# Optimization experiments

Measured on AMD Instinct MI355X. Metric: run time of the kernel, lower is better.

Reference implementation:

```python
import jax, jax.numpy as jnp
import numpy as np

# Dims: N=batch, C=heads (depthwise channels), H=W=seq_len (square causal map)
N, C, H, W = 2, 16, 2048, 2048
R, S = 6, 11            # kernel: R over out rows (queries), S over cols (keys)
PAD_H, PAD_W = 5, 5     # pad_h = R-1 (causal in h), pad_w = (S-1)//2 (centered in w)


def setup_inputs() -> dict:
    key = jax.random.key(0)
    k1, k2 = jax.random.split(key)
    x = jax.random.normal(k1, (N, C, H, W), dtype=jnp.float32)
    weight = jax.random.normal(k2, (C, R, S), dtype=jnp.float32) * 0.1
    return {"x": x, "weight": weight}


def reference(x, weight):
    # Causal (lower-triangular) mask h >= w, as in the Triton kernels'
    # `in_h >= in_w` / `out_h >= out_w` masking.
    causal_mask = jnp.tril(jnp.ones((H, W), dtype=bool))  # [H, W]

    # Mask input causally (matches bwd_weight masking x with in_h >= in_w).
    xm = jnp.where(causal_mask, x, jnp.zeros((), x.dtype))  # [N,C,H,W]

    # Depthwise cross-correlation:
    #   y[b,c,p,q] = sum_{r,s} w[c,r,s] * xm[b,c, p+r-PAD_H, q+s-PAD_W]
    # Asymmetric padding keeps output HxW: (PAD_H, R-1-PAD_H) in h => causal
    # taps p-(R-1)..p; (PAD_W, S-1-PAD_W) in w => centered taps.
    y = jax.lax.conv_general_dilated(
        xm,
        weight[:, None, :, :],  # [C,1,R,S] OIHW, depthwise via groups=C
        window_strides=(1, 1),
        padding=((PAD_H, R - 1 - PAD_H), (PAD_W, S - 1 - PAD_W)),
        dimension_numbers=("NCHW", "OIHW", "NCHW"),
        feature_group_count=C,
    )

    # Mask output causally (matches bwd_input masking dout with out_h >= out_w).
    return jnp.where(causal_mask, y, jnp.zeros((), y.dtype))
```

## Files before the change

kernel.cpp:

```cpp
#include <hip/hip_runtime.h>
#include <stdint.h>


#define HDIM 2048
#define WDIM 2048
#define CH   16

#define PITCH 88
#define XROWS 69
#define NSL   (XROWS * 20)

typedef float    f32x4 __attribute__((ext_vector_type(4)));
typedef _Float16 f16x8 __attribute__((ext_vector_type(8)));
typedef _Float16 f16x4 __attribute__((ext_vector_type(4)));

__global__ __launch_bounds__(256, 8)
void dwconv_mfma(const float* __restrict__ x, const float* __restrict__ wgt,
                 float* __restrict__ out) {
  const int bx = blockIdx.x, by = blockIdx.y, plane = blockIdx.z;
  const int q0 = bx * 64, p0 = by * 64;
  const int tid = threadIdx.x;
  const size_t pb = (size_t)plane * HDIM * WDIM;
  const float* __restrict__ xp = x + pb;
  float* __restrict__ op = out + pb;

  if (p0 + 63 < q0) {
    const float4 z = make_float4(0.f, 0.f, 0.f, 0.f);
#pragma unroll
    for (int i = 0; i < 4; ++i) {
      int idx = i * 256 + tid;
      int row = idx >> 4, c4 = idx & 15;
      *(float4*)(op + (size_t)(p0 + row) * WDIM + q0 + 4 * c4) = z;
    }
    return;
  }

  __shared__ _Float16 s_x[XROWS * PITCH];

  const bool pure = (bx >= 1) && (bx <= 30) && (p0 >= q0 + 76);
#pragma unroll
  for (int j = 0; j < 6; ++j) {
    int slot = j * 256 + tid;
    if (slot < NSL) {
      int row = slot / 20;
      int c4 = slot - row * 20;
      int ih = p0 - 5 + row;
      int cb = q0 - 8 + 4 * c4;
      float4 v = make_float4(0.f, 0.f, 0.f, 0.f);
      if (pure) {
        v = *(const float4*)(xp + (size_t)ih * WDIM + cb);
      } else if (ih >= 0) {
        bool fullv = (cb >= 0) && (cb + 3 <= ih) && (cb + 3 < WDIM);
        if (fullv) {
          v = *(const float4*)(xp + (size_t)ih * WDIM + cb);
        } else {
          float* vv = &v.x;
#pragma unroll
          for (int e = 0; e < 4; ++e) {
            int iw = cb + e;
            if (iw >= 0 && iw < WDIM && iw <= ih)
              vv[e] = xp[(size_t)ih * WDIM + iw];
          }
        }
      }
      f16x4 h4;
      h4[0] = (_Float16)v.x; h4[1] = (_Float16)v.y;
      h4[2] = (_Float16)v.z; h4[3] = (_Float16)v.w;
      *(f16x4*)&s_x[row * PITCH + 4 * c4] = h4;
    }
  }

  const int lane = tid & 63;
  const int j16 = lane & 15;
  const int wk = lane >> 4;
  const float* __restrict__ wcp = wgt + (plane & (CH - 1)) * 66;
  f16x8 bw[6];
#pragma unroll
  for (int r = 0; r < 6; ++r) {
#pragma unroll
    for (int i = 0; i < 8; ++i) {
      int k = 8 * wk + i;
      int d = k - j16 - 3;
      bw[r][i] = (_Float16)((d >= 0 && d <= 10) ? wcp[r * 11 + d] : 0.f);
    }
  }

  __syncthreads();

  const int wid = tid >> 6;
  f32x4 acc[4];
#pragma unroll
  for (int t = 0; t < 4; ++t) acc[t] = (f32x4){0.f, 0.f, 0.f, 0.f};

#pragma unroll
  for (int t = 0; t < 4; ++t) {
#pragma unroll
    for (int r = 0; r < 6; ++r) {
      int off = (16 * wid + j16 + r) * PITCH + 16 * t + 8 * wk;
      f16x8 ah = *(const f16x8*)&s_x[off];
      acc[t] = __builtin_amdgcn_mfma_f32_16x16x32_f16(ah, bw[r], acc[t], 0, 0, 0);
    }
  }

  const bool needmask = (q0 + 63 > p0);
#pragma unroll
  for (int t = 0; t < 4; ++t) {
    const int q = q0 + 16 * t + j16;
#pragma unroll
    for (int reg = 0; reg < 4; ++reg) {
      const int p = p0 + 16 * wid + 4 * wk + reg;
      float val = acc[t][reg];
      if (needmask && q > p) val = 0.f;
      op[(size_t)p * WDIM + q] = val;
    }
  }
}

extern "C" void kernel_launch(void* const* d_in, const int* in_sizes, int n_in,
                              void* d_out, int out_size, void* d_ws, size_t ws_size,
                              hipStream_t stream) {
  const float* x   = (const float*)d_in[0];
  const float* wgt = (const float*)d_in[1];
  float* out       = (float*)d_out;
  dim3 grid(WDIM / 64, HDIM / 64, 2 * CH);
  dwconv_mfma<<<grid, dim3(256), 0, stream>>>(x, wgt, out);
}
```

Before: 319.5 us.

## Process both batch planes per block, swap MFMA operands for float4 stores

Each block now handles the same channel for both batch elements. It stages two input tiles into shared memory and reuses the per-channel weight fragments, which halves the grid. The MFMA operands are swapped (weights as A, input as B), so each lane holds four consecutive output columns and can write them with one float4 store instead of scalar stores. Other changes: the shared pitch drops to 80, the f16 conversion uses packed cvt_pkrtz (round-toward-zero), and the launch-bounds occupancy hint is lowered to 6 to fit the larger shared footprint.

```diff
diff --git a/kernel.cpp b/kernel.cpp
--- a/kernel.cpp
+++ b/kernel.cpp
@@ -6,112 +6,130 @@
 #define WDIM 2048
 #define CH   16
 
-#define PITCH 88
+#define PITCH 80
 #define XROWS 69
 #define NSL   (XROWS * 20)
 
 typedef float    f32x4 __attribute__((ext_vector_type(4)));
+typedef __fp16   h16x2 __attribute__((ext_vector_type(2)));
 typedef _Float16 f16x8 __attribute__((ext_vector_type(8)));
-typedef _Float16 f16x4 __attribute__((ext_vector_type(4)));
 
-__global__ __launch_bounds__(256, 8)
+__global__ __launch_bounds__(256, 6)
 void dwconv_mfma(const float* __restrict__ x, const float* __restrict__ wgt,
                  float* __restrict__ out) {
-  const int bx = blockIdx.x, by = blockIdx.y, plane = blockIdx.z;
+  const int bx = blockIdx.x, by = blockIdx.y, zp = blockIdx.z;
   const int q0 = bx * 64, p0 = by * 64;
   const int tid = threadIdx.x;
-  const size_t pb = (size_t)plane * HDIM * WDIM;
-  const float* __restrict__ xp = x + pb;
-  float* __restrict__ op = out + pb;
+  const size_t pb0 = (size_t)zp * HDIM * WDIM;
+  const size_t pb1 = (size_t)(zp + CH) * HDIM * WDIM;
 
-  if (p0 + 63 < q0) {
+  if (by < bx) {
     const float4 z = make_float4(0.f, 0.f, 0.f, 0.f);
+    float* o0 = out + pb0 + (size_t)p0 * WDIM + q0;
+    float* o1 = out + pb1 + (size_t)p0 * WDIM + q0;
 #pragma unroll
     for (int i = 0; i < 4; ++i) {
       int idx = i * 256 + tid;
       int row = idx >> 4, c4 = idx & 15;
-      *(float4*)(op + (size_t)(p0 + row) * WDIM + q0 + 4 * c4) = z;
+      *(float4*)(o0 + (size_t)row * WDIM + 4 * c4) = z;
+      *(float4*)(o1 + (size_t)row * WDIM + 4 * c4) = z;
     }
     return;
   }
 
-  __shared__ _Float16 s_x[XROWS * PITCH];
+  __shared__ __attribute__((aligned(16))) _Float16 sx[2][XROWS * PITCH];
 
-  const bool pure = (bx >= 1) && (bx <= 30) && (p0 >= q0 + 76);
+  const bool pure = (bx >= 1) && (bx <= 30) && (by >= bx + 2);
+
+  auto stage_plane = [&](const float* __restrict__ xpl,
+                         _Float16* __restrict__ buf) {
 #pragma unroll
-  for (int j = 0; j < 6; ++j) {
-    int slot = j * 256 + tid;
-    if (slot < NSL) {
-      int row = slot / 20;
-      int c4 = slot - row * 20;
-      int ih = p0 - 5 + row;
-      int cb = q0 - 8 + 4 * c4;
-      float4 v = make_float4(0.f, 0.f, 0.f, 0.f);
-      if (pure) {
-        v = *(const float4*)(xp + (size_t)ih * WDIM + cb);
-      } else if (ih >= 0) {
-        bool fullv = (cb >= 0) && (cb + 3 <= ih) && (cb + 3 < WDIM);
-        if (fullv) {
-          v = *(const float4*)(xp + (size_t)ih * WDIM + cb);
-        } else {
-          float* vv = &v.x;
+    for (int j = 0; j < 6; ++j) {
+      int slot = j * 256 + tid;
+      if (slot < NSL) {
+        int row = slot / 20;
+        int c4 = slot - row * 20;
+        int ih = p0 - 5 + row;
+        int cb = q0 - 8 + 4 * c4;
+        float4 v = make_float4(0.f, 0.f, 0.f, 0.f);
+        if (pure) {
+          v = *(const float4*)(xpl + (size_t)ih * WDIM + cb);
+        } else if (ih >= 0) {
+          bool fullv = (cb >= 0) && (cb + 3 <= ih) && (cb + 3 < WDIM);
+          if (fullv) {
+            v = *(const float4*)(xpl + (size_t)ih * WDIM + cb);
+          } else {
+            float* vv = &v.x;
 #pragma unroll
-          for (int e = 0; e < 4; ++e) {
-            int iw = cb + e;
-            if (iw >= 0 && iw < WDIM && iw <= ih)
-              vv[e] = xp[(size_t)ih * WDIM + iw];
+            for (int e = 0; e < 4; ++e) {
+              int iw = cb + e;
+              if (iw >= 0 && iw < WDIM && iw <= ih)
+                vv[e] = xpl[(size_t)ih * WDIM + iw];
+            }
           }
         }
+        union { h16x2 h[2]; uint2 u; } cv;
+        cv.h[0] = __builtin_amdgcn_cvt_pkrtz(v.x, v.y);
+        cv.h[1] = __builtin_amdgcn_cvt_pkrtz(v.z, v.w);
+        *(uint2*)&buf[row * PITCH + 4 * c4] = cv.u;
       }
-      f16x4 h4;
-      h4[0] = (_Float16)v.x; h4[1] = (_Float16)v.y;
-      h4[2] = (_Float16)v.z; h4[3] = (_Float16)v.w;
-      *(f16x4*)&s_x[row * PITCH + 4 * c4] = h4;
     }
-  }
+  };
+
+  stage_plane(x + pb0, &sx[0][0]);
+  stage_plane(x + pb1, &sx[1][0]);
 
   const int lane = tid & 63;
   const int j16 = lane & 15;
-  const int wk = lane >> 4;
-  const float* __restrict__ wcp = wgt + (plane & (CH - 1)) * 66;
-  f16x8 bw[6];
+  const int wk  = lane >> 4;
+  const int wid = tid >> 6;
+  const float* __restrict__ wcp = wgt + zp * 66;
+  f16x8 aw[6];
 #pragma unroll
   for (int r = 0; r < 6; ++r) {
 #pragma unroll
     for (int i = 0; i < 8; ++i) {
-      int k = 8 * wk + i;
-      int d = k - j16 - 3;
-      bw[r][i] = (_Float16)((d >= 0 && d <= 10) ? wcp[r * 11 + d] : 0.f);
+      int d = 8 * wk + i - j16 - 3;
+      aw[r][i] = (_Float16)((d >= 0 && d <= 10) ? wcp[r * 11 + d] : 0.f);
     }
   }
 
   __syncthreads();
 
-  const int wid = tid >> 6;
-  f32x4 acc[4];
+  const bool dmask = (by == bx);
+
+#pragma unroll 1
+  for (int pl = 0; pl < 2; ++pl) {
+    const _Float16* __restrict__ lb = &sx[pl][0];
+    float* __restrict__ op = out + (pl ? pb1 : pb0);
+
+    f32x4 acc[4];
 #pragma unroll
-  for (int t = 0; t < 4; ++t) acc[t] = (f32x4){0.f, 0.f, 0.f, 0.f};
+    for (int qt = 0; qt < 4; ++qt) acc[qt] = (f32x4){0.f, 0.f, 0.f, 0.f};
 
 #pragma unroll
-  for (int t = 0; t < 4; ++t) {
+    for (int qt = 0; qt < 4; ++qt) {
 #pragma unroll
-    for (int r = 0; r < 6; ++r) {
-      int off = (16 * wid + j16 + r) * PITCH + 16 * t + 8 * wk;
-      f16x8 ah = *(const f16x8*)&s_x[off];
-      acc[t] = __builtin_amdgcn_mfma_f32_16x16x32_f16(ah, bw[r], acc[t], 0, 0, 0);
+      for (int r = 0; r < 6; ++r) {
+        int off = (16 * wid + j16 + r) * PITCH + 16 * qt + 8 * wk;
+        f16x8 xb = *(const f16x8*)&lb[off];
+        acc[qt] =
+            __builtin_amdgcn_mfma_f32_16x16x32_f16(aw[r], xb, acc[qt], 0, 0, 0);
+      }
     }
-  }
 
-  const bool needmask = (q0 + 63 > p0);
+    const int p = p0 + 16 * wid + j16;
 #pragma unroll
-  for (int t = 0; t < 4; ++t) {
-    const int q = q0 + 16 * t + j16;
+    for (int qt = 0; qt < 4; ++qt) {
+      const int q = q0 + 16 * qt + 4 * wk;
+      f32x4 a = acc[qt];
+      if (dmask) {
 #pragma unroll
-    for (int reg = 0; reg < 4; ++reg) {
-      const int p = p0 + 16 * wid + 4 * wk + reg;
-      float val = acc[t][reg];
-      if (needmask && q > p) val = 0.f;
-      op[(size_t)p * WDIM + q] = val;
+        for (int reg = 0; reg < 4; ++reg)
+          if (q + reg > p) a[reg] = 0.f;
+      }
+      *(float4*)(op + (size_t)p * WDIM + q) =
+          make_float4(a[0], a[1], a[2], a[3]);
     }
   }
 }
@@ -122,6 +140,6 @@
   const float* x   = (const float*)d_in[0];
   const float* wgt = (const float*)d_in[1];
   float* out       = (float*)d_out;
-  dim3 grid(WDIM / 64, HDIM / 64, 2 * CH);
+  dim3 grid(WDIM / 64, HDIM / 64, CH);
   dwconv_mfma<<<grid, dim3(256), 0, stream>>>(x, wgt, out);
 }
```

Result: slower. 334.3 us (+4.6%).
